# Optimization experiments

Measured on AMD Instinct MI355X. Metric: run time of the kernel, lower is better.

Reference implementation:

```python
import jax, jax.numpy as jnp
import numpy as np

N_HEADS = 12
VAL_DIM = 64
TOKEN_DIM = 768


def setup_inputs() -> dict:
    key = jax.random.key(0)
    k1, k2, k3 = jax.random.split(key, 3)
    x = jax.random.normal(k1, (8, 1024, TOKEN_DIM), dtype=jnp.float32)
    W_qkv = jax.random.normal(k2, (TOKEN_DIM, 3 * N_HEADS * VAL_DIM), dtype=jnp.float32) * (TOKEN_DIM ** -0.5)
    W_merge = jax.random.normal(k3, (N_HEADS * VAL_DIM, TOKEN_DIM), dtype=jnp.float32) * ((N_HEADS * VAL_DIM) ** -0.5)
    return {"x": x, "W_qkv": W_qkv, "W_merge": W_merge}


def reference(x, W_qkv, W_merge):
    b, p, _ = x.shape
    scale = VAL_DIM ** -0.5
    qkv = jnp.einsum('bpt,tf->bpf', x, W_qkv)  # (b, p, 3*h*v)
    # einops '(h v k)' -> k is innermost factor
    qkv = qkv.reshape(b, p, N_HEADS, VAL_DIM, 3)
    q = jnp.transpose(qkv[..., 0], (0, 2, 1, 3))  # (b, h, p, v)
    k = jnp.transpose(qkv[..., 1], (0, 2, 1, 3))
    v = jnp.transpose(qkv[..., 2], (0, 2, 1, 3))
    scores = jnp.einsum('bhid,bhjd->bhij', q, k) * scale
    attn = jax.nn.softmax(scores, axis=-1)
    out = jnp.einsum('bhij,bhjd->bhid', attn, v)
    out = jnp.transpose(out, (0, 2, 1, 3)).reshape(b, p, N_HEADS * VAL_DIM)
    return jnp.einsum('bpf,ft->bpt', out, W_merge)
```

## Files before the change

### kernel.cpp

```cpp
#include <hip/hip_runtime.h>
#include <hip/hip_bf16.h>
#include <math.h>


#define B_  8
#define P_  1024
#define T_  768
#define H_  12
#define DV  64
#define F3  2304
#define HD  768

typedef float  f32x4  __attribute__((ext_vector_type(4)));
typedef __bf16 bf16x4 __attribute__((ext_vector_type(4)));
typedef __bf16 bf16x8 __attribute__((ext_vector_type(8)));

#if defined(__has_builtin)
#if __has_builtin(__builtin_amdgcn_exp2f)
#define EX2(x) __builtin_amdgcn_exp2f(x)
#endif
#endif
#ifndef EX2
#define EX2(x) exp2f(x)
#endif

__device__ __forceinline__ void gload16(const void* g, void* l) {
    __builtin_amdgcn_global_load_lds((const __attribute__((address_space(1))) void*)g,
                                     (__attribute__((address_space(3))) void*)l,
                                     16, 0, 0);
}

__global__ __launch_bounds__(256) void k_prep(const float* __restrict__ x,
                                              __bf16* __restrict__ Xb,
                                              const float* __restrict__ wqkv,
                                              __bf16* __restrict__ WqT,
                                              const float* __restrict__ wm,
                                              __bf16* __restrict__ WmT) {
    int bid = blockIdx.x;
    int tid = threadIdx.x;

    if (bid < 768) {
        int xcd = bid & 7;
        int seq = bid >> 3;
        int strip = (seq / 12) * 8 + xcd;
        int sub   = seq % 12;
        size_t base = (size_t)strip * (128 * T_) + (size_t)sub * (128 * T_ / 12);
        const float4* s4 = (const float4*)(x + base);
        bf16x4*       d4 = (bf16x4*)(Xb + base);
#pragma unroll
        for (int i = 0; i < 8; i++) {
            float4 v = s4[i * 256 + tid];
            bf16x4 o = { (__bf16)v.x, (__bf16)v.y, (__bf16)v.z, (__bf16)v.w };
            d4[i * 256 + tid] = o;
        }
        return;
    }

    __shared__ __bf16 tile[32][33];
    int tx = tid & 31, ty = tid >> 5;

    if (bid < 768 + 1728) {
        int u  = bid - 768;
        int bx = u % 72, by = u / 72;
        int n = bx * 32 + tx;
        int r = n / 768, idx = n - r * 768;
        int f = (idx >> 6) * 192 + (idx & 63) * 3 + r;
        int t0 = by * 32;
#pragma unroll
        for (int j = 0; j < 32; j += 8)
            tile[ty + j][tx] = (__bf16)wqkv[(size_t)(t0 + ty + j) * F3 + f];
        __syncthreads();
#pragma unroll
        for (int j = 0; j < 32; j += 8)
            WqT[(size_t)(bx * 32 + ty + j) * T_ + t0 + tx] = tile[tx][ty + j];
    } else {
        int u  = bid - 768 - 1728;
        int bx = u % 24, by = u / 24;
        int xx = bx * 32 + tx;
        int y  = by * 32 + ty;
#pragma unroll
        for (int j = 0; j < 32; j += 8)
            tile[ty + j][tx] = (__bf16)wm[(size_t)(y + j) * HD + xx];
        __syncthreads();
        int x2 = by * 32 + tx;
        int y2 = bx * 32 + ty;
#pragma unroll
        for (int j = 0; j < 32; j += 8)
            WmT[(size_t)(y2 + j) * T_ + x2] = tile[tx][ty + j];
    }
}

#define GEMM64_MAINLOOP(Aptr, Btptr, brow, bcol, LD)                             \
    int tid  = threadIdx.x;                                                      \
    int lane = tid & 63, wave = tid >> 6;                                        \
    int l16  = lane & 15, quad = lane >> 4;                                      \
    int wm = (wave >> 1) * 64, wn = (wave & 1) * 64;                             \
    int bro = tid >> 3, bq = tid & 7;                                            \
    f32x4 acc[4][4];                                                             \
    _Pragma("unroll") for (int i = 0; i < 4; i++)                                \
        _Pragma("unroll") for (int j = 0; j < 4; j++)                            \
            acc[i][j] = (f32x4){0.f, 0.f, 0.f, 0.f};                             \
    _Pragma("unroll") for (int it = 0; it < 4; it++) {                           \
        int n = it * 32 + bro;                                                   \
        int gp = bq ^ (n & 7);                                                   \
        gload16((Aptr) + (size_t)((brow) * 128 + n) * (LD) + gp * 8,             \
                LDSb + it * 2048 + tid * 8);                                     \
        gload16((Btptr) + (size_t)((bcol) * 128 + n) * (LD) + gp * 8,            \
                LDSb + 8192 + it * 2048 + tid * 8);                              \
    }                                                                            \
    for (int k0 = 0; k0 < (LD); k0 += 64) {                                      \
        int cur = (k0 >> 6) & 1;                                                 \
        __bf16* As = LDSb + cur * 16384;                                         \
        __bf16* Bs = As + 8192;                                                  \
        if (k0 + 64 < (LD)) {                                                    \
            __bf16* Ad = LDSb + (cur ^ 1) * 16384;                               \
            _Pragma("unroll") for (int it = 0; it < 4; it++) {                   \
                int n = it * 32 + bro;                                           \
                int gp = bq ^ (n & 7);                                           \
                gload16((Aptr) + (size_t)((brow) * 128 + n) * (LD) + k0 + 64 + gp * 8, \
                        Ad + it * 2048 + tid * 8);                               \
                gload16((Btptr) + (size_t)((bcol) * 128 + n) * (LD) + k0 + 64 + gp * 8, \
                        Ad + 8192 + it * 2048 + tid * 8);                        \
            }                                                                    \
            asm volatile("s_waitcnt vmcnt(8)" ::: "memory");                     \
        } else {                                                                 \
            asm volatile("s_waitcnt vmcnt(0)" ::: "memory");                     \
        }                                                                        \
        __builtin_amdgcn_s_barrier();                                            \
        _Pragma("unroll") for (int ks = 0; ks < 2; ks++) {                       \
            bf16x8 af[4], bfr[4];                                                \
            _Pragma("unroll") for (int i = 0; i < 4; i++) {                      \
                int r = wm + i * 16 + l16;                                       \
                af[i] = *(const bf16x8*)&As[r * 64 + (((ks * 4 + quad) ^ (r & 7)) << 3)]; \
            }                                                                    \
            _Pragma("unroll") for (int j = 0; j < 4; j++) {                      \
                int r = wn + j * 16 + l16;                                       \
                bfr[j] = *(const bf16x8*)&Bs[r * 64 + (((ks * 4 + quad) ^ (r & 7)) << 3)]; \
            }                                                                    \
            _Pragma("unroll") for (int i = 0; i < 4; i++)                        \
                _Pragma("unroll") for (int j = 0; j < 4; j++)                    \
                    acc[i][j] = __builtin_amdgcn_mfma_f32_16x16x32_bf16(         \
                        af[i], bfr[j], acc[i][j], 0, 0, 0);                      \
        }                                                                        \
        __builtin_amdgcn_s_barrier();                                            \
    }

__global__ __launch_bounds__(256, 2) void k_qkv(const __bf16* __restrict__ Xb,
                                                const __bf16* __restrict__ Wt,
                                                __bf16* __restrict__ Q,
                                                __bf16* __restrict__ K,
                                                __bf16* __restrict__ Vt) {
    __shared__ __align__(16) __bf16 LDSb[2 * 2 * 128 * 64];

    int bid  = blockIdx.x;
    int xcd  = bid & 7;
    int seq  = bid >> 3;
    int chunk = seq / 48;
    int rem   = seq - chunk * 48;
    int brow  = (rem / 6) * 8 + xcd;
    int bcol  = chunk * 6 + (rem % 6);

    GEMM64_MAINLOOP(Xb, Wt, brow, bcol, T_)

    int region = chunk;
    int b  = brow >> 3;
    int p0 = (brow & 7) * 128;
    int bcl = bcol - region * 6;

    if (region < 2) {
        __bf16* D = region == 0 ? Q : K;
        float sc = region == 0 ? 0.1803368801f : 1.0f;
        __syncthreads();
#pragma unroll
        for (int i = 0; i < 4; i++) {
            int m_loc = wm + i * 16 + quad * 4;
#pragma unroll
            for (int j = 0; j < 4; j++) {
                int n_loc = wn + j * 16 + l16;
#pragma unroll
                for (int r = 0; r < 4; r++) {
                    int m = m_loc + r;
                    int phys = (n_loc >> 3) ^ (m & 15);
                    LDSb[m * 128 + phys * 8 + (n_loc & 7)] =
                        (__bf16)(acc[i][j][r] * sc);
                }
            }
        }
        __syncthreads();
        int m_loc = tid >> 1;
        int halfn = tid & 1;
        size_t prow = (size_t)(p0 + m_loc);
#pragma unroll
        for (int i = 0; i < 8; i++) {
            int ch   = halfn * 8 + i;
            int phys = ch ^ (m_loc & 15);
            bf16x8 val = *(const bf16x8*)&LDSb[m_loc * 128 + phys * 8];
            int f = bcl * 128 + ch * 8;
            int h = f >> 6, v = f & 63;
            __bf16* Dh = D + ((size_t)(b * H_ + h) * P_ + prow) * DV + v;
            *(bf16x8*)Dh = val;
        }
    } else {
        __syncthreads();
#pragma unroll
        for (int j = 0; j < 4; j++) {
            int n_loc = wn + j * 16 + l16;
#pragma unroll
            for (int i = 0; i < 4; i++)
#pragma unroll
            for (int r = 0; r < 4; r++) {
                int m_loc = wm + i * 16 + quad * 4 + r;
                int phys  = (m_loc >> 3) ^ (n_loc & 15);
                LDSb[n_loc * 128 + phys * 8 + (m_loc & 7)] = (__bf16)acc[i][j][r];
            }
        }
        __syncthreads();
        int n_loc = tid >> 1, halfm = tid & 1;
        int idx = bcl * 128 + n_loc;
        int h = idx >> 6, v = idx & 63;
        __bf16* Dh = Vt + ((size_t)(b * H_ + h) * DV + v) * P_ + p0 + halfm * 64;
#pragma unroll
        for (int i = 0; i < 8; i++) {
            int chunk2 = halfm * 8 + i;
            int phys   = chunk2 ^ (n_loc & 15);
            bf16x8 val = *(const bf16x8*)&LDSb[n_loc * 128 + phys * 8];
            *(bf16x8*)(Dh + i * 8) = val;
        }
    }
}

__global__ __launch_bounds__(256, 2) void k_merge(const __bf16* __restrict__ O,
                                                  const __bf16* __restrict__ Wt,
                                                  float* __restrict__ out) {
    __shared__ __align__(16) __bf16 LDSb[2 * 2 * 128 * 64];

    int bid  = blockIdx.x;
    int xcd  = bid & 7;
    int seq  = bid >> 3;
    int brow = (seq / 6) * 8 + xcd;
    int bcol = seq % 6;

    GEMM64_MAINLOOP(O, Wt, brow, bcol, HD)

#pragma unroll
    for (int i = 0; i < 4; i++)
#pragma unroll
        for (int j = 0; j < 4; j++) {
            int col = bcol * 128 + wn + j * 16 + l16;
#pragma unroll
            for (int r = 0; r < 4; r++) {
                size_t row = (size_t)(brow * 128 + wm + i * 16 + quad * 4 + r);
                out[row * HD + col] = acc[i][j][r];
            }
        }
}

__global__ __launch_bounds__(256, 3) void k_attn(const __bf16* __restrict__ Q,
                                                 const __bf16* __restrict__ Kb,
                                                 const __bf16* __restrict__ Vt,
                                                 __bf16* __restrict__ O) {
    __shared__ __align__(16) __bf16 KV[2][8192];

    int tid  = threadIdx.x;
    int lane = tid & 63, wave = tid >> 6;
    int l16  = lane & 15, quad = lane >> 4;

    int bid = blockIdx.x;
    int xcd = bid & 7;
    int seq = bid >> 3;
    int bh  = xcd * 12 + (seq % 12);
    int qt  = seq / 12;
    int b   = bh / H_, h = bh % H_;

    const __bf16* Qb  = Q  + (size_t)bh * P_ * DV;
    const __bf16* Kbh = Kb + (size_t)bh * P_ * DV;
    const __bf16* Vbh = Vt + (size_t)bh * DV * P_;
    int m0 = qt * 128 + wave * 32;

    bf16x8 a00 = *(const bf16x8*)(Qb + (size_t)(m0 + l16) * DV + quad * 8);
    bf16x8 a01 = *(const bf16x8*)(Qb + (size_t)(m0 + l16) * DV + 32 + quad * 8);
    bf16x8 a10 = *(const bf16x8*)(Qb + (size_t)(m0 + 16 + l16) * DV + quad * 8);
    bf16x8 a11 = *(const bf16x8*)(Qb + (size_t)(m0 + 16 + l16) * DV + 32 + quad * 8);

    int l8 = lane >> 3, q8 = lane & 7;

    bf16x8 ones;
#pragma unroll
    for (int i = 0; i < 8; i++) ones[i] = (__bf16)1.0f;

    f32x4 facc0 = {0.f,0.f,0.f,0.f}, facc1 = {0.f,0.f,0.f,0.f};
    f32x4 oacc0[4] = {{0.f,0.f,0.f,0.f},{0.f,0.f,0.f,0.f},{0.f,0.f,0.f,0.f},{0.f,0.f,0.f,0.f}};
    f32x4 oacc1[4] = {{0.f,0.f,0.f,0.f},{0.f,0.f,0.f,0.f},{0.f,0.f,0.f,0.f},{0.f,0.f,0.f,0.f}};
    int swq = l16 & 7;

#pragma unroll
    for (int i = 0; i < 2; i++) {
        int t8 = wave * 2 + i;
        int r  = t8 * 8 + l8;
        int j  = q8 ^ (r & 7);
        gload16(Kbh + (size_t)r * DV + j * 8, &KV[0][t8 * 512 + lane * 8]);
        gload16(Vbh + (size_t)r * P_ + j * 8, &KV[0][4096 + t8 * 512 + lane * 8]);
    }

    for (int t = 0; t < 16; t++) {
        int cur = t & 1;
        const __bf16* Ks = &KV[cur][0];
        const __bf16* Vs = &KV[cur][4096];

        if (t < 15) {
            __bf16* Kd = &KV[cur ^ 1][0];
            int c = (t + 1) * 64;
#pragma unroll
            for (int i = 0; i < 2; i++) {
                int t8 = wave * 2 + i;
                int r  = t8 * 8 + l8;
                int j  = q8 ^ (r & 7);
                gload16(Kbh + (size_t)(c + r) * DV + j * 8, Kd + t8 * 512 + lane * 8);
                gload16(Vbh + (size_t)r * P_ + c + j * 8,  Kd + 4096 + t8 * 512 + lane * 8);
            }
            asm volatile("s_waitcnt vmcnt(4)" ::: "memory");
        } else {
            asm volatile("s_waitcnt vmcnt(0)" ::: "memory");
        }
        __builtin_amdgcn_s_barrier();

        f32x4 s0[4], s1[4];
#pragma unroll
        for (int ct = 0; ct < 4; ct++) {
            int R = ct * 16 + l16;
            bf16x8 b0 = *(const bf16x8*)&Ks[R * 64 + ((quad ^ swq) * 8)];
            bf16x8 b1 = *(const bf16x8*)&Ks[R * 64 + (((4 + quad) ^ swq) * 8)];
            f32x4 z0 = {0.f, 0.f, 0.f, 0.f};
            z0 = __builtin_amdgcn_mfma_f32_16x16x32_bf16(b0, a00, z0, 0, 0, 0);
            z0 = __builtin_amdgcn_mfma_f32_16x16x32_bf16(b1, a01, z0, 0, 0, 0);
            s0[ct] = z0;
            f32x4 z1 = {0.f, 0.f, 0.f, 0.f};
            z1 = __builtin_amdgcn_mfma_f32_16x16x32_bf16(b0, a10, z1, 0, 0, 0);
            z1 = __builtin_amdgcn_mfma_f32_16x16x32_bf16(b1, a11, z1, 0, 0, 0);
            s1[ct] = z1;
        }

#pragma unroll
        for (int ks = 0; ks < 2; ks++) {
            bf16x8 pf0, pf1;
#pragma unroll
            for (int r = 0; r < 4; r++) {
                pf0[r]     = (__bf16)EX2(s0[2 * ks][r]);
                pf0[4 + r] = (__bf16)EX2(s0[2 * ks + 1][r]);
                pf1[r]     = (__bf16)EX2(s1[2 * ks][r]);
                pf1[4 + r] = (__bf16)EX2(s1[2 * ks + 1][r]);
            }
            facc0 = __builtin_amdgcn_mfma_f32_16x16x32_bf16(ones, pf0, facc0, 0, 0, 0);
            facc1 = __builtin_amdgcn_mfma_f32_16x16x32_bf16(ones, pf1, facc1, 0, 0, 0);
            int c8lo = (4 * ks + (quad >> 1)) ^ swq;
            int c8hi = (4 * ks + 2 + (quad >> 1)) ^ swq;
            int halfo = (quad & 1) << 2;
#pragma unroll
            for (int nt = 0; nt < 4; nt++) {
                const __bf16* row = &Vs[(nt * 16 + l16) * 64];
                bf16x4 lo = *(const bf16x4*)&row[c8lo * 8 + halfo];
                bf16x4 hi = *(const bf16x4*)&row[c8hi * 8 + halfo];
                bf16x8 av = {lo[0], lo[1], lo[2], lo[3],
                             hi[0], hi[1], hi[2], hi[3]};
                oacc0[nt] = __builtin_amdgcn_mfma_f32_16x16x32_bf16(av, pf0, oacc0[nt], 0, 0, 0);
                oacc1[nt] = __builtin_amdgcn_mfma_f32_16x16x32_bf16(av, pf1, oacc1[nt], 0, 0, 0);
            }
        }
        __builtin_amdgcn_s_barrier();
    }

    float inv0 = 1.0f / facc0[0];
    float inv1 = 1.0f / facc1[0];

    {
        int p = m0 + l16;
        __bf16* Orow = O + ((size_t)b * P_ + p) * HD + h * DV;
#pragma unroll
        for (int nt = 0; nt < 4; nt++) {
            bf16x4 o4;
#pragma unroll
            for (int r = 0; r < 4; r++) o4[r] = (__bf16)(oacc0[nt][r] * inv0);
            *(bf16x4*)&Orow[nt * 16 + quad * 4] = o4;
        }
    }
    {
        int p = m0 + 16 + l16;
        __bf16* Orow = O + ((size_t)b * P_ + p) * HD + h * DV;
#pragma unroll
        for (int nt = 0; nt < 4; nt++) {
            bf16x4 o4;
#pragma unroll
            for (int r = 0; r < 4; r++) o4[r] = (__bf16)(oacc1[nt][r] * inv1);
            *(bf16x4*)&Orow[nt * 16 + quad * 4] = o4;
        }
    }
}

extern "C" void kernel_launch(void* const* d_in, const int* in_sizes, int n_in,
                              void* d_out, int out_size, void* d_ws, size_t ws_size,
                              hipStream_t stream) {
    const float* x      = (const float*)d_in[0];
    const float* wqkv   = (const float*)d_in[1];
    const float* wmerge = (const float*)d_in[2];

    char* w = (char*)d_ws;
    __bf16* Xb  = (__bf16*)w;  w += (size_t)B_ * P_ * T_ * 2;
    __bf16* WqT = (__bf16*)w;  w += (size_t)F3 * T_ * 2;
    __bf16* WmT = (__bf16*)w;  w += (size_t)HD * T_ * 2;
    __bf16* Q   = (__bf16*)w;  w += (size_t)B_ * H_ * P_ * DV * 2;
    __bf16* K   = (__bf16*)w;  w += (size_t)B_ * H_ * P_ * DV * 2;
    __bf16* Vt  = (__bf16*)w;  w += (size_t)B_ * H_ * P_ * DV * 2;
    __bf16* O   = (__bf16*)w;

    hipLaunchKernelGGL(k_prep, dim3(768 + 1728 + 576), dim3(256), 0, stream,
                       x, Xb, wqkv, WqT, wmerge, WmT);

    hipLaunchKernelGGL(k_qkv, dim3((B_ * P_ / 128) * (F3 / 128)), dim3(256), 0, stream,
                       Xb, WqT, Q, K, Vt);

    hipLaunchKernelGGL(k_attn, dim3(B_ * H_ * (P_ / 128)), dim3(256), 0, stream,
                       Q, K, Vt, O);

    hipLaunchKernelGGL(k_merge, dim3((B_ * P_ / 128) * (HD / 128)), dim3(256), 0, stream,
                       O, WmT, (float*)d_out);
}
```

Before: 171.1 us.

## Enlarge QKV GEMM tile to 256x128 with 512-thread blocks

The QKV projection kernel now computes a 256x128 output tile per block using 8 waves instead of a 128x128 tile with 4 waves, which halves the grid. The main loop is inlined with a larger double-buffered LDS allocation, and the V-transpose epilogue is changed to handle 256-row tiles. The intent is to reuse each loaded weight tile across more rows and cut global and LDS traffic per FLOP. In exchange, each block uses much more LDS, which may lower the number of resident blocks per CU and change how evenly the work spreads across CUs.

```diff
diff --git a/kernel.cpp b/kernel.cpp
--- a/kernel.cpp
+++ b/kernel.cpp
@@ -145,27 +145,102 @@
         __builtin_amdgcn_s_barrier();                                            \
     }
 
-__global__ __launch_bounds__(256, 2) void k_qkv(const __bf16* __restrict__ Xb,
+__global__ __launch_bounds__(512, 2) void k_qkv(const __bf16* __restrict__ Xb,
                                                 const __bf16* __restrict__ Wt,
                                                 __bf16* __restrict__ Q,
                                                 __bf16* __restrict__ K,
                                                 __bf16* __restrict__ Vt) {
-    __shared__ __align__(16) __bf16 LDSb[2 * 2 * 128 * 64];
+    __shared__ __align__(16) __bf16 LDSb[2 * 24576];
 
     int bid  = blockIdx.x;
     int xcd  = bid & 7;
     int seq  = bid >> 3;
-    int chunk = seq / 48;
-    int rem   = seq - chunk * 48;
-    int brow  = (rem / 6) * 8 + xcd;
-    int bcol  = chunk * 6 + (rem % 6);
-
-    GEMM64_MAINLOOP(Xb, Wt, brow, bcol, T_)
+    int chunk = seq / 24;
+    int rem   = seq - chunk * 24;
+    int browt = (rem / 6) * 8 + xcd;
+    int bcolt = chunk * 6 + (rem % 6);
+
+    int tid  = threadIdx.x;
+    int lane = tid & 63, wave = tid >> 6;
+    int l16  = lane & 15, quad = lane >> 4;
+    int wm = (wave >> 1) * 64;
+    int wn = (wave & 1) * 64;
+    int r8 = tid >> 3, bq = tid & 7;
+
+    f32x4 acc[4][4];
+#pragma unroll
+    for (int i = 0; i < 4; i++)
+#pragma unroll
+        for (int j = 0; j < 4; j++)
+            acc[i][j] = (f32x4){0.f, 0.f, 0.f, 0.f};
+
+#pragma unroll
+    for (int it = 0; it < 4; it++) {
+        int r = it * 64 + r8;
+        int gp = bq ^ (r & 7);
+        gload16(Xb + (size_t)(browt * 256 + r) * T_ + gp * 8,
+                LDSb + it * 4096 + tid * 8);
+    }
+#pragma unroll
+    for (int it = 0; it < 2; it++) {
+        int r = it * 64 + r8;
+        int gp = bq ^ (r & 7);
+        gload16(Wt + (size_t)(bcolt * 128 + r) * T_ + gp * 8,
+                LDSb + 16384 + it * 4096 + tid * 8);
+    }
+
+    for (int k0 = 0; k0 < T_; k0 += 64) {
+        int cur = (k0 >> 6) & 1;
+        __bf16* As = LDSb + cur * 24576;
+        __bf16* Bs = As + 16384;
+        if (k0 + 64 < T_) {
+            __bf16* Ad = LDSb + (cur ^ 1) * 24576;
+#pragma unroll
+            for (int it = 0; it < 4; it++) {
+                int r = it * 64 + r8;
+                int gp = bq ^ (r & 7);
+                gload16(Xb + (size_t)(browt * 256 + r) * T_ + k0 + 64 + gp * 8,
+                        Ad + it * 4096 + tid * 8);
+            }
+#pragma unroll
+            for (int it = 0; it < 2; it++) {
+                int r = it * 64 + r8;
+                int gp = bq ^ (r & 7);
+                gload16(Wt + (size_t)(bcolt * 128 + r) * T_ + k0 + 64 + gp * 8,
+                        Ad + 16384 + it * 4096 + tid * 8);
+            }
+            asm volatile("s_waitcnt vmcnt(6)" ::: "memory");
+        } else {
+            asm volatile("s_waitcnt vmcnt(0)" ::: "memory");
+        }
+        __builtin_amdgcn_s_barrier();
+#pragma unroll
+        for (int ks = 0; ks < 2; ks++) {
+            bf16x8 af[4], bfr[4];
+#pragma unroll
+            for (int i = 0; i < 4; i++) {
+                int r = wm + i * 16 + l16;
+                af[i] = *(const bf16x8*)&As[r * 64 + (((ks * 4 + quad) ^ (r & 7)) << 3)];
+            }
+#pragma unroll
+            for (int j = 0; j < 4; j++) {
+                int r = wn + j * 16 + l16;
+                bfr[j] = *(const bf16x8*)&Bs[r * 64 + (((ks * 4 + quad) ^ (r & 7)) << 3)];
+            }
+#pragma unroll
+            for (int i = 0; i < 4; i++)
+#pragma unroll
+                for (int j = 0; j < 4; j++)
+                    acc[i][j] = __builtin_amdgcn_mfma_f32_16x16x32_bf16(
+                        af[i], bfr[j], acc[i][j], 0, 0, 0);
+        }
+        __builtin_amdgcn_s_barrier();
+    }
 
     int region = chunk;
-    int b  = brow >> 3;
-    int p0 = (brow & 7) * 128;
-    int bcl = bcol - region * 6;
+    int b  = browt >> 2;
+    int p0 = (browt & 3) * 256;
+    int bcl = bcolt - region * 6;
 
     if (region < 2) {
         __bf16* D = region == 0 ? Q : K;
@@ -173,13 +248,13 @@
         __syncthreads();
 #pragma unroll
         for (int i = 0; i < 4; i++) {
-            int m_loc = wm + i * 16 + quad * 4;
+            int m_base = wm + i * 16 + quad * 4;
 #pragma unroll
             for (int j = 0; j < 4; j++) {
                 int n_loc = wn + j * 16 + l16;
 #pragma unroll
                 for (int r = 0; r < 4; r++) {
-                    int m = m_loc + r;
+                    int m = m_base + r;
                     int phys = (n_loc >> 3) ^ (m & 15);
                     LDSb[m * 128 + phys * 8 + (n_loc & 7)] =
                         (__bf16)(acc[i][j][r] * sc);
@@ -210,20 +285,21 @@
 #pragma unroll
             for (int r = 0; r < 4; r++) {
                 int m_loc = wm + i * 16 + quad * 4 + r;
-                int phys  = (m_loc >> 3) ^ (n_loc & 15);
-                LDSb[n_loc * 128 + phys * 8 + (m_loc & 7)] = (__bf16)acc[i][j][r];
+                int phys  = (m_loc >> 3) ^ (n_loc & 31);
+                LDSb[n_loc * 256 + phys * 8 + (m_loc & 7)] = (__bf16)acc[i][j][r];
             }
         }
         __syncthreads();
-        int n_loc = tid >> 1, halfm = tid & 1;
+        int n_loc = tid >> 2;
+        int qm    = tid & 3;
         int idx = bcl * 128 + n_loc;
         int h = idx >> 6, v = idx & 63;
-        __bf16* Dh = Vt + ((size_t)(b * H_ + h) * DV + v) * P_ + p0 + halfm * 64;
+        __bf16* Dh = Vt + ((size_t)(b * H_ + h) * DV + v) * P_ + p0 + qm * 64;
 #pragma unroll
         for (int i = 0; i < 8; i++) {
-            int chunk2 = halfm * 8 + i;
-            int phys   = chunk2 ^ (n_loc & 15);
-            bf16x8 val = *(const bf16x8*)&LDSb[n_loc * 128 + phys * 8];
+            int ch2  = qm * 8 + i;
+            int phys = ch2 ^ (n_loc & 31);
+            bf16x8 val = *(const bf16x8*)&LDSb[n_loc * 256 + phys * 8];
             *(bf16x8*)(Dh + i * 8) = val;
         }
     }
@@ -415,7 +491,7 @@
     hipLaunchKernelGGL(k_prep, dim3(768 + 1728 + 576), dim3(256), 0, stream,
                        x, Xb, wqkv, WqT, wmerge, WmT);
 
-    hipLaunchKernelGGL(k_qkv, dim3((B_ * P_ / 128) * (F3 / 128)), dim3(256), 0, stream,
+    hipLaunchKernelGGL(k_qkv, dim3(576), dim3(512), 0, stream,
                        Xb, WqT, Q, K, Vt);
 
     hipLaunchKernelGGL(k_attn, dim3(B_ * H_ * (P_ / 128)), dim3(256), 0, stream,
```

After: 179.4 us. +4.8%, slower.
